# Kernel tuning notes

Measured on AMD Instinct MI355X. Metric: run time of the kernel, lower is better.

## Reference

```python
import jax, jax.numpy as jnp
import numpy as np

EPS = 1e-7
IOU_THRESHOLD = 0.5
PENALTY_FACTOR = 0.1
BOX_LOSS_WEIGHT = 5.0
OBJ_LOSS_WEIGHT = 1.0
SMALL_OBJ_SCALE = 2.0
SMALL_SIZE_THRESHOLD = 0.05


def _xywh_to_xyxy(b):
    return jnp.concatenate([b[..., :2] - b[..., 2:] / 2, b[..., :2] + b[..., 2:] / 2], axis=-1)


def _bbox_ciou(box1, box2, eps=EPS):
    # box1, box2: (..., 4) in xyxy format
    b1_x1, b1_y1, b1_x2, b1_y2 = box1[..., 0], box1[..., 1], box1[..., 2], box1[..., 3]
    b2_x1, b2_y1, b2_x2, b2_y2 = box2[..., 0], box2[..., 1], box2[..., 2], box2[..., 3]
    b1_area = (b1_x2 - b1_x1) * (b1_y2 - b1_y1)
    b2_area = (b2_x2 - b2_x1) * (b2_y2 - b2_y1)
    inter_w = jnp.clip(jnp.minimum(b1_x2, b2_x2) - jnp.maximum(b1_x1, b2_x1), 0)
    inter_h = jnp.clip(jnp.minimum(b1_y2, b2_y2) - jnp.maximum(b1_y1, b2_y1), 0)
    inter_area = inter_w * inter_h
    union_area = b1_area + b2_area - inter_area + eps
    iou = inter_area / union_area
    c2 = (jnp.maximum(b1_x2, b2_x2) - jnp.minimum(b1_x1, b2_x1)) ** 2 + \
         (jnp.maximum(b1_y2, b2_y2) - jnp.minimum(b1_y1, b2_y1)) ** 2 + eps
    center_dist2 = ((b1_x1 + b1_x2) / 2 - (b2_x1 + b2_x2) / 2) ** 2 + \
                   ((b1_y1 + b1_y2) / 2 - (b2_y1 + b2_y2) / 2) ** 2
    w1, h1 = b1_x2 - b1_x1, b1_y2 - b1_y1
    w2, h2 = b2_x2 - b2_x1, b2_y2 - b2_y1
    v = (4.0 / (jnp.pi ** 2)) * (jnp.arctan(w1 / (h1 + eps)) - jnp.arctan(w2 / (h2 + eps))) ** 2
    alpha = v / (1 - iou + v + eps)
    return iou - (center_dist2 / c2 + alpha * v)


def setup_inputs() -> dict:
    key = jax.random.key(0)
    k0, k1, k2, k3, k4 = jax.random.split(key, 5)
    B, Np, Ng, C = 16, 8192, 128, 80
    return {
        "batch_y_hat": jax.random.uniform(k0, (B, Np, 4), dtype=jnp.float32),
        "batch_y": jax.random.uniform(k1, (B, Ng, 4), dtype=jnp.float32),
        "batch_obj_scores": jax.random.normal(k2, (B, Np), dtype=jnp.float32),
        "batch_class_pred": jax.random.normal(k3, (B, Np, C), dtype=jnp.float32),
        "batch_class_target": jax.random.randint(k4, (B, Ng), 0, C),
        "min_obj_score": 0,
    }


def reference(batch_y_hat, batch_y, batch_obj_scores, batch_class_pred, batch_class_target, min_obj_score):
    valid = batch_obj_scores > min_obj_score                      # (B, Np) kept predictions
    p = _xywh_to_xyxy(batch_y_hat)                                # (B, Np, 4)
    g = _xywh_to_xyxy(batch_y)                                    # (B, Ng, 4)
    # pairwise IoU (xywh compute_iou, which has no eps)
    lt = jnp.maximum(p[:, :, None, :2], g[:, None, :, :2])       # (B, Np, Ng, 2)
    rb = jnp.minimum(p[:, :, None, 2:], g[:, None, :, 2:])
    wh = jnp.clip(rb - lt, 0)
    inter = wh[..., 0] * wh[..., 1]                               # (B, Np, Ng)
    area_p = (p[..., 2] - p[..., 0]) * (p[..., 3] - p[..., 1])
    area_g = (g[..., 2] - g[..., 0]) * (g[..., 3] - g[..., 1])
    iou_mat = inter / (area_p[:, :, None] + area_g[:, None, :] - inter)
    max_iou = jnp.max(iou_mat, axis=-1)                           # (B, Np)
    match_idx = jnp.argmax(iou_mat, axis=-1)                      # (B, Np)
    matched = valid & (max_iou > IOU_THRESHOLD)
    unmatched = valid & ~matched
    # CIoU localization loss over matched preds
    matched_gt_xyxy = jnp.take_along_axis(g, match_idx[..., None], axis=1)   # (B, Np, 4)
    ciou_loss = 1.0 - _bbox_ciou(p, matched_gt_xyxy)              # (B, Np)
    is_small = (batch_y[..., 2] < SMALL_SIZE_THRESHOLD) | (batch_y[..., 3] < SMALL_SIZE_THRESHOLD)  # (B, Ng)
    w_small = jnp.where(jnp.take_along_axis(is_small, match_idx, axis=1), SMALL_OBJ_SCALE, 1.0)
    n_match = jnp.sum(matched, axis=1)
    loc_loss = jnp.where(n_match > 0,
                         jnp.sum(ciou_loss * w_small * matched, axis=1) / jnp.maximum(n_match, 1),
                         0.0)
    # classification loss over matched preds
    logp = jax.nn.log_softmax(batch_class_pred, axis=-1)          # (B, Np, C)
    tgt = jnp.take_along_axis(batch_class_target, match_idx, axis=1)
    ce = -jnp.take_along_axis(logp, tgt[..., None], axis=-1)[..., 0]
    cls_loss = jnp.where(n_match > 0,
                         jnp.sum(ce * w_small * matched, axis=1) / jnp.maximum(n_match, 1),
                         0.0)
    # penalty on unmatched objectness scores
    penalty = PENALTY_FACTOR * jnp.sum(batch_obj_scores * unmatched, axis=1)
    # objectness BCE-with-logits over valid preds, FN reweighted x2
    s = batch_obj_scores
    lbl = matched.astype(s.dtype)
    bce = jnp.clip(s, 0) - s * lbl + jnp.log1p(jnp.exp(-jnp.abs(s)))
    w_obj = jnp.where(matched & (s < 0.5), 2.0, 1.0)
    n_valid = jnp.sum(valid, axis=1)
    obj_loss = jnp.where(n_valid > 0,
                         jnp.sum(bce * w_obj * valid, axis=1) / jnp.maximum(n_valid, 1),
                         0.0)
    per_batch = BOX_LOSS_WEIGHT * loc_loss + OBJ_LOSS_WEIGHT * obj_loss + penalty + cls_loss
    valid_b = n_valid > 0
    n_vb = jnp.sum(valid_b)
    return jnp.sum(jnp.where(valid_b, per_batch, 0.0)) / jnp.maximum(n_vb, 1)
```

## Files before the change

kernel.cpp:

```cpp
#include <hip/hip_runtime.h>
#include <math.h>

#define B_  16
#define NP_ 8192
#define NG_ 128
#define NC_ 80
#define PPB_ 128
#define NBX_ (NP_ / PPB_)

#define EPS_       1e-7f
#define IOU_THR_   0.5f
#define PEN_       0.1f
#define BOXW_      5.0f
#define SMALLSC_   2.0f
#define SMALLTH_   0.05f


__global__ __launch_bounds__(256) void yolo_main(
    const float* __restrict__ y_hat,
    const float* __restrict__ ygt,
    const float* __restrict__ obj,
    const float* __restrict__ clsp,
    const int*   __restrict__ tgt,
    const int*   __restrict__ min_s,
    float* __restrict__ part)
{
    __shared__ float4 g4[NG_];
    __shared__ float  garea[NG_], gws[NG_];
    __shared__ int    gtc[NG_];
    __shared__ float  mbuf[PPB_][4];
    __shared__ float  wred[4][6];

    const int b    = blockIdx.y;
    const int tid  = threadIdx.x;
    const int pl   = tid & (PPB_ - 1);
    const int half = tid >> 7;
    const int p    = blockIdx.x * PPB_ + pl;

    if (tid < NG_) {
        float4 gb = *(const float4*)(ygt + ((size_t)b * NG_ + tid) * 4);
        float x1 = gb.x - gb.z * 0.5f, y1 = gb.y - gb.w * 0.5f;
        float x2 = gb.x + gb.z * 0.5f, y2 = gb.y + gb.w * 0.5f;
        g4[tid] = make_float4(x1, y1, x2, y2);
        garea[tid] = (x2 - x1) * (y2 - y1);
        gws[tid]   = ((gb.z < SMALLTH_) || (gb.w < SMALLTH_)) ? SMALLSC_ : 1.0f;
        gtc[tid]   = tgt[b * NG_ + tid];
    }
    __syncthreads();

    const float min_score = (float)min_s[0];

    float4 pb = *(const float4*)(y_hat + ((size_t)b * NP_ + p) * 4);
    float px1 = pb.x - pb.z * 0.5f, py1 = pb.y - pb.w * 0.5f;
    float px2 = pb.x + pb.z * 0.5f, py2 = pb.y + pb.w * 0.5f;
    float area_p = (px2 - px1) * (py2 - py1);

    float bi_inter = -1.0f, bi_union = 1.0f;
    int   bi = half * 64;
    const int j0 = half * 64;
    #pragma unroll 8
    for (int jj = 0; jj < 64; ++jj) {
        int j = j0 + jj;
        float4 g = g4[j];
        float w = fmaxf(fminf(px2, g.z) - fmaxf(px1, g.x), 0.0f);
        float h = fmaxf(fminf(py2, g.w) - fmaxf(py1, g.y), 0.0f);
        float inter = w * h;
        float uni = area_p + garea[j] - inter;
        bool better = inter * bi_union > bi_inter * uni;
        bi_inter = better ? inter : bi_inter;
        bi_union = better ? uni   : bi_union;
        bi       = better ? j     : bi;
    }

    if (half == 1) {
        mbuf[pl][0] = bi_inter;
        mbuf[pl][1] = bi_union;
        mbuf[pl][2] = (float)bi;
    }
    __syncthreads();

    float f_loc = 0.f, f_ce = 0.f, f_pen = 0.f, f_bce = 0.f, n_m = 0.f, n_v = 0.f;

    if (half == 0) {
        float oi = mbuf[pl][0], ou = mbuf[pl][1];
        if (oi * bi_union > bi_inter * ou) {
            bi_inter = oi; bi_union = ou; bi = (int)mbuf[pl][2];
        }
        float max_iou = bi_inter / bi_union;

        float s = obj[(size_t)b * NP_ + p];
        bool valid     = s > min_score;
        bool matched   = valid && (max_iou > IOU_THR_);
        bool unmatched = valid && !matched;

        n_m = matched ? 1.f : 0.f;
        n_v = valid   ? 1.f : 0.f;
        if (unmatched) f_pen = PEN_ * s;

        if (valid) {
            float lbl = matched ? 1.f : 0.f;
            float bce = fmaxf(s, 0.f) - s * lbl + log1pf(expf(-fabsf(s)));
            float w_obj = (matched && s < 0.5f) ? 2.f : 1.f;
            f_bce = bce * w_obj;
        }

        if (matched) {
            float wsm = gws[bi];
            float4 g = g4[bi];
            float bx1 = g.x, by1 = g.y, bx2 = g.z, by2 = g.w;
            float b1a = (px2 - px1) * (py2 - py1);
            float b2a = (bx2 - bx1) * (by2 - by1);
            float iw = fmaxf(fminf(px2, bx2) - fmaxf(px1, bx1), 0.f);
            float ih = fmaxf(fminf(py2, by2) - fmaxf(py1, by1), 0.f);
            float inter = iw * ih;
            float uni = b1a + b2a - inter + EPS_;
            float iou = inter / uni;
            float cw = fmaxf(px2, bx2) - fminf(px1, bx1);
            float ch = fmaxf(py2, by2) - fminf(py1, by1);
            float c2 = cw * cw + ch * ch + EPS_;
            float dx = (px1 + px2) * 0.5f - (bx1 + bx2) * 0.5f;
            float dy = (py1 + py2) * 0.5f - (by1 + by2) * 0.5f;
            float rho2 = dx * dx + dy * dy;
            float w1 = px2 - px1, h1 = py2 - py1;
            float w2 = bx2 - bx1, h2 = by2 - by1;
            float dat = atanf(w1 / (h1 + EPS_)) - atanf(w2 / (h2 + EPS_));
            float v = (float)(4.0 / (M_PI * M_PI)) * dat * dat;
            float alpha = v / (1.f - iou + v + EPS_);
            float ciou = iou - (rho2 / c2 + alpha * v);
            f_loc = (1.f - ciou) * wsm;

            const float* row = clsp + ((size_t)b * NP_ + p) * NC_;
            float m = -INFINITY;
            #pragma unroll
            for (int k = 0; k < NC_ / 4; ++k) {
                float4 v4 = ((const float4*)row)[k];
                m = fmaxf(m, fmaxf(fmaxf(v4.x, v4.y), fmaxf(v4.z, v4.w)));
            }
            float se = 0.f;
            #pragma unroll
            for (int k = 0; k < NC_ / 4; ++k) {
                float4 v4 = ((const float4*)row)[k];
                se += expf(v4.x - m) + expf(v4.y - m) + expf(v4.z - m) + expf(v4.w - m);
            }
            int t = gtc[bi];
            float ce = -(row[t] - m - logf(se));
            f_ce = ce * wsm;
        }
    }

    float vals[6] = { n_m, n_v, f_loc, f_ce, f_pen, f_bce };
    #pragma unroll
    for (int i = 0; i < 6; ++i) {
        float v = vals[i];
        #pragma unroll
        for (int off = 32; off > 0; off >>= 1)
            v += __shfl_down(v, off, 64);
        vals[i] = v;
    }
    int wave = tid >> 6, lane = tid & 63;
    if (lane == 0) {
        #pragma unroll
        for (int i = 0; i < 6; ++i) wred[wave][i] = vals[i];
    }
    __syncthreads();
    if (tid == 0) {
        float* slot = part + ((size_t)b * NBX_ + blockIdx.x) * 6;
        #pragma unroll
        for (int i = 0; i < 6; ++i)
            slot[i] = wred[0][i] + wred[1][i] + wred[2][i] + wred[3][i];
    }
}

__global__ __launch_bounds__(64) void yolo_final(const float* __restrict__ part,
                                                 float* __restrict__ out)
{
    int lane = threadIdx.x;
    int b    = lane >> 2;
    int sub  = lane & 3;

    float v[6] = {0.f, 0.f, 0.f, 0.f, 0.f, 0.f};
    for (int k = 0; k < NBX_ / 4; ++k) {
        const float* slot = part + ((size_t)b * NBX_ + sub + 4 * k) * 6;
        #pragma unroll
        for (int i = 0; i < 6; ++i) v[i] += slot[i];
    }
    #pragma unroll
    for (int i = 0; i < 6; ++i) {
        v[i] += __shfl_xor(v[i], 1, 64);
        v[i] += __shfl_xor(v[i], 2, 64);
    }

    float pbv = 0.f, cnt = 0.f;
    if (sub == 0) {
        float nm = v[0], nv = v[1];
        float loc = nm > 0.f ? v[2] / nm : 0.f;
        float ce  = nm > 0.f ? v[3] / nm : 0.f;
        float ob  = nv > 0.f ? v[5] / nv : 0.f;
        float per = BOXW_ * loc + ob + v[4] + ce;
        if (nv > 0.f) { pbv = per; cnt = 1.f; }
    }
    #pragma unroll
    for (int off = 32; off > 0; off >>= 1) {
        pbv += __shfl_down(pbv, off, 64);
        cnt += __shfl_down(cnt, off, 64);
    }
    if (lane == 0) out[0] = pbv / fmaxf(cnt, 1.f);
}

extern "C" void kernel_launch(void* const* d_in, const int* in_sizes, int n_in,
                              void* d_out, int out_size, void* d_ws, size_t ws_size,
                              hipStream_t stream) {
    const float* y_hat = (const float*)d_in[0];
    const float* ygt   = (const float*)d_in[1];
    const float* obj   = (const float*)d_in[2];
    const float* clsp  = (const float*)d_in[3];
    const int*   tgt   = (const int*)d_in[4];
    const int*   mins  = (const int*)d_in[5];
    float* part = (float*)d_ws;
    float* out  = (float*)d_out;

    dim3 grid(NBX_, B_);
    yolo_main<<<grid, 256, 0, stream>>>(y_hat, ygt, obj, clsp, tgt, mins, part);
    yolo_final<<<1, 64, 0, stream>>>(part, out);
}
```

Before: 106.0 us.

## Split GT matching across four waves per 64 predictions and drop block reduction

Each block now handles 64 predictions, and its four waves each scan a quarter of the 128 GT boxes rather than two halves of 128 predictions. The partial best matches are merged through shared memory by wave 0, which alone runs the loss tail. Its single-wave shuffle reduction writes the partial sums directly, removing the cross-wave shared reduction and the final barrier. This shortens the serial IoU loop per thread and doubles the block count, at the cost of re-loading the GT table per block and leaving three waves idle during the tail and the softmax work.

After: 105.6 us. Within noise of the previous version (-0.3%).

```diff
diff --git a/kernel.cpp b/kernel.cpp
--- a/kernel.cpp
+++ b/kernel.cpp
@@ -5,7 +5,7 @@
 #define NP_ 8192
 #define NG_ 128
 #define NC_ 80
-#define PPB_ 128
+#define PPB_ 64
 #define NBX_ (NP_ / PPB_)
 
 #define EPS_       1e-7f
@@ -28,14 +28,13 @@
     __shared__ float4 g4[NG_];
     __shared__ float  garea[NG_], gws[NG_];
     __shared__ int    gtc[NG_];
-    __shared__ float  mbuf[PPB_][4];
-    __shared__ float  wred[4][6];
-
-    const int b    = blockIdx.y;
-    const int tid  = threadIdx.x;
-    const int pl   = tid & (PPB_ - 1);
-    const int half = tid >> 7;
-    const int p    = blockIdx.x * PPB_ + pl;
+    __shared__ float4 mbuf[3][PPB_];
+
+    const int b   = blockIdx.y;
+    const int tid = threadIdx.x;
+    const int pl  = tid & 63;
+    const int q   = tid >> 6;
+    const int p   = blockIdx.x * PPB_ + pl;
 
     if (tid < NG_) {
         float4 gb = *(const float4*)(ygt + ((size_t)b * NG_ + tid) * 4);
@@ -56,10 +55,10 @@
     float area_p = (px2 - px1) * (py2 - py1);
 
     float bi_inter = -1.0f, bi_union = 1.0f;
-    int   bi = half * 64;
-    const int j0 = half * 64;
+    const int j0 = q * 32;
+    int bi = j0;
     #pragma unroll 8
-    for (int jj = 0; jj < 64; ++jj) {
+    for (int jj = 0; jj < 32; ++jj) {
         int j = j0 + jj;
         float4 g = g4[j];
         float w = fmaxf(fminf(px2, g.z) - fmaxf(px1, g.x), 0.0f);
@@ -72,80 +71,77 @@
         bi       = better ? j     : bi;
     }
 
-    if (half == 1) {
-        mbuf[pl][0] = bi_inter;
-        mbuf[pl][1] = bi_union;
-        mbuf[pl][2] = (float)bi;
-    }
+    if (q != 0) mbuf[q - 1][pl] = make_float4(bi_inter, bi_union, (float)bi, 0.f);
     __syncthreads();
-
-    float f_loc = 0.f, f_ce = 0.f, f_pen = 0.f, f_bce = 0.f, n_m = 0.f, n_v = 0.f;
-
-    if (half == 0) {
-        float oi = mbuf[pl][0], ou = mbuf[pl][1];
-        if (oi * bi_union > bi_inter * ou) {
-            bi_inter = oi; bi_union = ou; bi = (int)mbuf[pl][2];
+    if (q != 0) return;
+
+    #pragma unroll
+    for (int k = 0; k < 3; ++k) {
+        float4 o = mbuf[k][pl];
+        if (o.x * bi_union > bi_inter * o.y) {
+            bi_inter = o.x; bi_union = o.y; bi = (int)o.z;
         }
-        float max_iou = bi_inter / bi_union;
-
-        float s = obj[(size_t)b * NP_ + p];
-        bool valid     = s > min_score;
-        bool matched   = valid && (max_iou > IOU_THR_);
-        bool unmatched = valid && !matched;
-
-        n_m = matched ? 1.f : 0.f;
-        n_v = valid   ? 1.f : 0.f;
-        if (unmatched) f_pen = PEN_ * s;
-
-        if (valid) {
-            float lbl = matched ? 1.f : 0.f;
-            float bce = fmaxf(s, 0.f) - s * lbl + log1pf(expf(-fabsf(s)));
-            float w_obj = (matched && s < 0.5f) ? 2.f : 1.f;
-            f_bce = bce * w_obj;
+    }
+    float max_iou = bi_inter / bi_union;
+
+    float s = obj[(size_t)b * NP_ + p];
+    bool valid     = s > min_score;
+    bool matched   = valid && (max_iou > IOU_THR_);
+    bool unmatched = valid && !matched;
+
+    float f_loc = 0.f, f_ce = 0.f, f_pen = 0.f, f_bce = 0.f;
+    float n_m = matched ? 1.f : 0.f;
+    float n_v = valid   ? 1.f : 0.f;
+    if (unmatched) f_pen = PEN_ * s;
+
+    if (valid) {
+        float lbl = matched ? 1.f : 0.f;
+        float bce = fmaxf(s, 0.f) - s * lbl + log1pf(expf(-fabsf(s)));
+        float w_obj = (matched && s < 0.5f) ? 2.f : 1.f;
+        f_bce = bce * w_obj;
+    }
+
+    if (matched) {
+        float wsm = gws[bi];
+        float4 g = g4[bi];
+        float bx1 = g.x, by1 = g.y, bx2 = g.z, by2 = g.w;
+        float b1a = (px2 - px1) * (py2 - py1);
+        float b2a = (bx2 - bx1) * (by2 - by1);
+        float iw = fmaxf(fminf(px2, bx2) - fmaxf(px1, bx1), 0.f);
+        float ih = fmaxf(fminf(py2, by2) - fmaxf(py1, by1), 0.f);
+        float inter = iw * ih;
+        float uni = b1a + b2a - inter + EPS_;
+        float iou = inter / uni;
+        float cw = fmaxf(px2, bx2) - fminf(px1, bx1);
+        float ch = fmaxf(py2, by2) - fminf(py1, by1);
+        float c2 = cw * cw + ch * ch + EPS_;
+        float dx = (px1 + px2) * 0.5f - (bx1 + bx2) * 0.5f;
+        float dy = (py1 + py2) * 0.5f - (by1 + by2) * 0.5f;
+        float rho2 = dx * dx + dy * dy;
+        float w1 = px2 - px1, h1 = py2 - py1;
+        float w2 = bx2 - bx1, h2 = by2 - by1;
+        float dat = atanf(w1 / (h1 + EPS_)) - atanf(w2 / (h2 + EPS_));
+        float v = (float)(4.0 / (M_PI * M_PI)) * dat * dat;
+        float alpha = v / (1.f - iou + v + EPS_);
+        float ciou = iou - (rho2 / c2 + alpha * v);
+        f_loc = (1.f - ciou) * wsm;
+
+        const float* row = clsp + ((size_t)b * NP_ + p) * NC_;
+        float m = -INFINITY;
+        #pragma unroll
+        for (int k = 0; k < NC_ / 4; ++k) {
+            float4 v4 = ((const float4*)row)[k];
+            m = fmaxf(m, fmaxf(fmaxf(v4.x, v4.y), fmaxf(v4.z, v4.w)));
         }
-
-        if (matched) {
-            float wsm = gws[bi];
-            float4 g = g4[bi];
-            float bx1 = g.x, by1 = g.y, bx2 = g.z, by2 = g.w;
-            float b1a = (px2 - px1) * (py2 - py1);
-            float b2a = (bx2 - bx1) * (by2 - by1);
-            float iw = fmaxf(fminf(px2, bx2) - fmaxf(px1, bx1), 0.f);
-            float ih = fmaxf(fminf(py2, by2) - fmaxf(py1, by1), 0.f);
-            float inter = iw * ih;
-            float uni = b1a + b2a - inter + EPS_;
-            float iou = inter / uni;
-            float cw = fmaxf(px2, bx2) - fminf(px1, bx1);
-            float ch = fmaxf(py2, by2) - fminf(py1, by1);
-            float c2 = cw * cw + ch * ch + EPS_;
-            float dx = (px1 + px2) * 0.5f - (bx1 + bx2) * 0.5f;
-            float dy = (py1 + py2) * 0.5f - (by1 + by2) * 0.5f;
-            float rho2 = dx * dx + dy * dy;
-            float w1 = px2 - px1, h1 = py2 - py1;
-            float w2 = bx2 - bx1, h2 = by2 - by1;
-            float dat = atanf(w1 / (h1 + EPS_)) - atanf(w2 / (h2 + EPS_));
-            float v = (float)(4.0 / (M_PI * M_PI)) * dat * dat;
-            float alpha = v / (1.f - iou + v + EPS_);
-            float ciou = iou - (rho2 / c2 + alpha * v);
-            f_loc = (1.f - ciou) * wsm;
-
-            const float* row = clsp + ((size_t)b * NP_ + p) * NC_;
-            float m = -INFINITY;
-            #pragma unroll
-            for (int k = 0; k < NC_ / 4; ++k) {
-                float4 v4 = ((const float4*)row)[k];
-                m = fmaxf(m, fmaxf(fmaxf(v4.x, v4.y), fmaxf(v4.z, v4.w)));
-            }
-            float se = 0.f;
-            #pragma unroll
-            for (int k = 0; k < NC_ / 4; ++k) {
-                float4 v4 = ((const float4*)row)[k];
-                se += expf(v4.x - m) + expf(v4.y - m) + expf(v4.z - m) + expf(v4.w - m);
-            }
-            int t = gtc[bi];
-            float ce = -(row[t] - m - logf(se));
-            f_ce = ce * wsm;
+        float se = 0.f;
+        #pragma unroll
+        for (int k = 0; k < NC_ / 4; ++k) {
+            float4 v4 = ((const float4*)row)[k];
+            se += expf(v4.x - m) + expf(v4.y - m) + expf(v4.z - m) + expf(v4.w - m);
         }
+        int t = gtc[bi];
+        float ce = -(row[t] - m - logf(se));
+        f_ce = ce * wsm;
     }
 
     float vals[6] = { n_m, n_v, f_loc, f_ce, f_pen, f_bce };
@@ -157,17 +153,10 @@
             v += __shfl_down(v, off, 64);
         vals[i] = v;
     }
-    int wave = tid >> 6, lane = tid & 63;
-    if (lane == 0) {
-        #pragma unroll
-        for (int i = 0; i < 6; ++i) wred[wave][i] = vals[i];
-    }
-    __syncthreads();
-    if (tid == 0) {
+    if (pl == 0) {
         float* slot = part + ((size_t)b * NBX_ + blockIdx.x) * 6;
         #pragma unroll
-        for (int i = 0; i < 6; ++i)
-            slot[i] = wred[0][i] + wred[1][i] + wred[2][i] + wred[3][i];
+        for (int i = 0; i < 6; ++i) slot[i] = vals[i];
     }
 }
 
```
